# Optimization experiments

Measured on AMD Instinct MI355X. Metric: run time of the kernel, lower is better.

## Reference

```python
import jax, jax.numpy as jnp
import numpy as np

EPS = 1e-8
TWO_PI = 2.0 * np.pi


def diff_round(x):
    # differentiable soft-round used for mask sharpening
    return x - jnp.sin(TWO_PI * x) / TWO_PI


def setup_inputs() -> dict:
    key = jax.random.key(0)
    k1, k2 = jax.random.split(key)
    B, N, P, Q = 8, 16384, 8, 8  # batch, superpixel areas, patch h, patch w
    sv_area_image = jax.random.normal(k1, (B, N, P, Q), dtype=jnp.float32)
    sv_area_mask = jax.random.uniform(k2, (B, N, P, Q), dtype=jnp.float32)
    return {"sv_area_image": sv_area_image, "sv_area_mask": sv_area_mask}


def reference(sv_area_image, sv_area_mask):
    # reshaped_mask = diff_round(diff_round(mask)) as in get_area_loss
    m = diff_round(diff_round(sv_area_mask))
    # per-area masked mean / variance (get_single_area_loss, doubly vmapped)
    masked = sv_area_image * m                      # [B, N, P, Q]
    msum = jnp.sum(m, axis=(-2, -1)) + EPS          # [B, N]
    mean = jnp.sum(masked, axis=(-2, -1)) / msum    # [B, N]
    dev = (masked - mean[..., None, None]) * m      # [B, N, P, Q]
    varr = jnp.sum(dev * dev, axis=(-2, -1)) / msum # [B, N]
    return jnp.mean(varr)
```

## Files before the change

kernel.cpp:

```cpp
#include <hip/hip_runtime.h>

#define TPB 256
#define MAX_BLOCKS 2048

__device__ __forceinline__ float sin2pi(float x) {
    return __builtin_amdgcn_sinf(x);
}

__device__ __forceinline__ float diff_round(float x) {
    return __builtin_fmaf(sin2pi(x), -0.15915494309189533577f, x);
}

template <int CTRL>
__device__ __forceinline__ float dpp_add(float v) {
    int i = __float_as_int(v);
    int m = __builtin_amdgcn_update_dpp(i, i, CTRL, 0xF, 0xF, false);
    return v + __int_as_float(m);
}

__device__ __forceinline__ float row_sum16(float s) {
    s = dpp_add<0xB1>(s);
    s = dpp_add<0x4E>(s);
    s = dpp_add<0x124>(s);
    s = dpp_add<0x128>(s);
    return s;
}

__device__ __forceinline__ float tile_varr(const float4 iv, const float4 mv) {
    float m0 = diff_round(diff_round(mv.x));
    float m1 = diff_round(diff_round(mv.y));
    float m2 = diff_round(diff_round(mv.z));
    float m3 = diff_round(diff_round(mv.w));
    float x0 = iv.x * m0, x1 = iv.y * m1, x2 = iv.z * m2, x3 = iv.w * m3;

    float sm = row_sum16((m0 + m1) + (m2 + m3));
    float sx = row_sum16((x0 + x1) + (x2 + x3));
    const float inv_msum = __builtin_amdgcn_rcpf(sm + 1e-8f);
    const float mean = sx * inv_msum;

    float d0 = (x0 - mean) * m0;
    float d1 = (x1 - mean) * m1;
    float d2 = (x2 - mean) * m2;
    float d3 = (x3 - mean) * m3;
    float sd = row_sum16((d0 * d0 + d1 * d1) + (d2 * d2 + d3 * d3));
    return sd * inv_msum;
}

__device__ __forceinline__ void load_pair(const float* __restrict__ img,
                                          const float* __restrict__ msk,
                                          int t0, int ntiles, int j,
                                          float4& ivA, float4& mvA,
                                          float4& ivB, float4& mvB) {
    ivA = mvA = ivB = mvB = make_float4(0.f, 0.f, 0.f, 0.f);
    const size_t off = (size_t)t0 * 64 + (size_t)j * 4;
    if (t0 < ntiles) {
        ivA = *reinterpret_cast<const float4*>(img + off);
        mvA = *reinterpret_cast<const float4*>(msk + off);
    }
    if (t0 + 1 < ntiles) {
        ivB = *reinterpret_cast<const float4*>(img + off + 64);
        mvB = *reinterpret_cast<const float4*>(msk + off + 64);
    }
}

__global__ __launch_bounds__(TPB) void area_var_partial(
    const float* __restrict__ img, const float* __restrict__ msk,
    float* __restrict__ partial, int ntiles) {
    const int tid  = threadIdx.x;
    const int wave = tid >> 6;
    const int lane = tid & 63;
    const int grp  = lane >> 4;
    const int j    = lane & 15;

    const int tiles_per_block = (TPB / 64) * 4 * 2;
    const int stride = gridDim.x * tiles_per_block;
    int t0 = blockIdx.x * tiles_per_block + (wave * 4 + grp) * 2;

    float acc = 0.0f;
    if (t0 < ntiles) {
        float4 ivA, mvA, ivB, mvB;
        load_pair(img, msk, t0, ntiles, j, ivA, mvA, ivB, mvB);
        for (;;) {
            const int nt = t0 + stride;
            const bool more = nt < ntiles;
            float4 nivA, nmvA, nivB, nmvB;
            nivA = nmvA = nivB = nmvB = make_float4(0.f, 0.f, 0.f, 0.f);
            if (more)
                load_pair(img, msk, nt, ntiles, j, nivA, nmvA, nivB, nmvB);
            acc += tile_varr(ivA, mvA);
            acc += tile_varr(ivB, mvB);
            if (!more) break;
            ivA = nivA; mvA = nmvA; ivB = nivB; mvB = nmvB; t0 = nt;
        }
    }
    acc += __shfl_xor(acc, 16, 64);
    acc += __shfl_xor(acc, 32, 64);

    __shared__ float wsum[TPB / 64];
    if (lane == 0) wsum[wave] = acc;
    __syncthreads();
    if (tid == 0) partial[blockIdx.x] = (wsum[0] + wsum[1]) + (wsum[2] + wsum[3]);
}

__global__ __launch_bounds__(TPB) void final_reduce(
    const float* __restrict__ partial, float* __restrict__ out,
    int n, float inv_count) {
    float s = 0.f;
    for (int i = threadIdx.x; i < n; i += TPB) s += partial[i];
    #pragma unroll
    for (int d = 1; d < 64; d <<= 1) s += __shfl_xor(s, d, 64);
    __shared__ float wsum[TPB / 64];
    const int wave = threadIdx.x >> 6;
    const int lane = threadIdx.x & 63;
    if (lane == 0) wsum[wave] = s;
    __syncthreads();
    if (threadIdx.x == 0)
        out[0] = ((wsum[0] + wsum[1]) + (wsum[2] + wsum[3])) * inv_count;
}

extern "C" void kernel_launch(void* const* d_in, const int* in_sizes, int n_in,
                              void* d_out, int out_size, void* d_ws, size_t ws_size,
                              hipStream_t stream) {
    const float* img = (const float*)d_in[0];
    const float* msk = (const float*)d_in[1];
    float* out = (float*)d_out;
    float* partial = (float*)d_ws;

    const int ntiles = in_sizes[0] / 64;
    int nblocks = (ntiles + 31) / 32;
    if (nblocks > MAX_BLOCKS) nblocks = MAX_BLOCKS;

    area_var_partial<<<nblocks, TPB, 0, stream>>>(img, msk, partial, ntiles);
    final_reduce<<<1, TPB, 0, stream>>>(partial, out, nblocks,
                                        1.0f / (float)ntiles);
}
```

Measured before the change: 94.26 us.

## Compute variance in one pass from moment sums and drop software prefetch

Replaces the two-pass per-tile variance (mean, then squared masked deviations) with a single pass that accumulates five moment sums (sum m, sum x, sum u^2, sum u*m, sum m^2) and combines them algebraically. This removes the dependency of the second reduction on the first, so all five DPP row-reductions can issue together. It also drops the manual double-buffered prefetch in favour of a plain grid-stride loop and adds an occupancy hint of 8 blocks per CU in launch bounds. In exchange it uses more DPP reductions per tile, and the one-pass formula can lose precision through cancellation.

```diff
diff --git a/kernel.cpp b/kernel.cpp
--- a/kernel.cpp
+++ b/kernel.cpp
@@ -26,44 +26,36 @@
     return s;
 }
 
-__device__ __forceinline__ float tile_varr(const float4 iv, const float4 mv) {
-    float m0 = diff_round(diff_round(mv.x));
-    float m1 = diff_round(diff_round(mv.y));
-    float m2 = diff_round(diff_round(mv.z));
-    float m3 = diff_round(diff_round(mv.w));
-    float x0 = iv.x * m0, x1 = iv.y * m1, x2 = iv.z * m2, x3 = iv.w * m3;
+struct Sums { float s1, sx, a, b, c; };
 
-    float sm = row_sum16((m0 + m1) + (m2 + m3));
-    float sx = row_sum16((x0 + x1) + (x2 + x3));
-    const float inv_msum = __builtin_amdgcn_rcpf(sm + 1e-8f);
-    const float mean = sx * inv_msum;
-
-    float d0 = (x0 - mean) * m0;
-    float d1 = (x1 - mean) * m1;
-    float d2 = (x2 - mean) * m2;
-    float d3 = (x3 - mean) * m3;
-    float sd = row_sum16((d0 * d0 + d1 * d1) + (d2 * d2 + d3 * d3));
-    return sd * inv_msum;
+__device__ __forceinline__ void accum(Sums& s, float i, float mraw) {
+    const float m = diff_round(diff_round(mraw));
+    const float x = i * m;
+    const float u = x * m;
+    s.s1 += m;
+    s.sx += x;
+    s.a = __builtin_fmaf(u, u, s.a);
+    s.b = __builtin_fmaf(u, m, s.b);
+    s.c = __builtin_fmaf(m, m, s.c);
 }
 
-__device__ __forceinline__ void load_pair(const float* __restrict__ img,
-                                          const float* __restrict__ msk,
-                                          int t0, int ntiles, int j,
-                                          float4& ivA, float4& mvA,
-                                          float4& ivB, float4& mvB) {
-    ivA = mvA = ivB = mvB = make_float4(0.f, 0.f, 0.f, 0.f);
-    const size_t off = (size_t)t0 * 64 + (size_t)j * 4;
-    if (t0 < ntiles) {
-        ivA = *reinterpret_cast<const float4*>(img + off);
-        mvA = *reinterpret_cast<const float4*>(msk + off);
-    }
-    if (t0 + 1 < ntiles) {
-        ivB = *reinterpret_cast<const float4*>(img + off + 64);
-        mvB = *reinterpret_cast<const float4*>(msk + off + 64);
-    }
+__device__ __forceinline__ float tile_varr(const float4 iv, const float4 mv) {
+    Sums s = {0.f, 0.f, 0.f, 0.f, 0.f};
+    accum(s, iv.x, mv.x);
+    accum(s, iv.y, mv.y);
+    accum(s, iv.z, mv.z);
+    accum(s, iv.w, mv.w);
+    const float S1 = row_sum16(s.s1);
+    const float Sx = row_sum16(s.sx);
+    const float A  = row_sum16(s.a);
+    const float B  = row_sum16(s.b);
+    const float C  = row_sum16(s.c);
+    const float r    = __builtin_amdgcn_rcpf(S1 + 1e-8f);
+    const float mean = Sx * r;
+    return __builtin_fmaf(-mean, __builtin_fmaf(-mean, C, 2.0f * B), A) * r;
 }
 
-__global__ __launch_bounds__(TPB) void area_var_partial(
+__global__ __launch_bounds__(TPB, 8) void area_var_partial(
     const float* __restrict__ img, const float* __restrict__ msk,
     float* __restrict__ partial, int ntiles) {
     const int tid  = threadIdx.x;
@@ -74,25 +66,23 @@
 
     const int tiles_per_block = (TPB / 64) * 4 * 2;
     const int stride = gridDim.x * tiles_per_block;
-    int t0 = blockIdx.x * tiles_per_block + (wave * 4 + grp) * 2;
+    float acc = 0.0f;
 
-    float acc = 0.0f;
-    if (t0 < ntiles) {
-        float4 ivA, mvA, ivB, mvB;
-        load_pair(img, msk, t0, ntiles, j, ivA, mvA, ivB, mvB);
-        for (;;) {
-            const int nt = t0 + stride;
-            const bool more = nt < ntiles;
-            float4 nivA, nmvA, nivB, nmvB;
-            nivA = nmvA = nivB = nmvB = make_float4(0.f, 0.f, 0.f, 0.f);
-            if (more)
-                load_pair(img, msk, nt, ntiles, j, nivA, nmvA, nivB, nmvB);
-            acc += tile_varr(ivA, mvA);
-            acc += tile_varr(ivB, mvB);
-            if (!more) break;
-            ivA = nivA; mvA = nmvA; ivB = nivB; mvB = nmvB; t0 = nt;
+    for (int t0 = blockIdx.x * tiles_per_block + (wave * 4 + grp) * 2;
+         t0 < ntiles; t0 += stride) {
+        const size_t off = (size_t)t0 * 64 + (size_t)j * 4;
+        const float4 ivA = *reinterpret_cast<const float4*>(img + off);
+        const float4 mvA = *reinterpret_cast<const float4*>(msk + off);
+        float4 ivB = make_float4(0.f, 0.f, 0.f, 0.f);
+        float4 mvB = make_float4(0.f, 0.f, 0.f, 0.f);
+        if (t0 + 1 < ntiles) {
+            ivB = *reinterpret_cast<const float4*>(img + off + 64);
+            mvB = *reinterpret_cast<const float4*>(msk + off + 64);
         }
+        acc += tile_varr(ivA, mvA);
+        acc += tile_varr(ivB, mvB);
     }
+
     acc += __shfl_xor(acc, 16, 64);
     acc += __shfl_xor(acc, 32, 64);
 
```

Result: no change. 94.54 us (median of 2 runs) (+0.3%).
